# Kernel tuning notes

Measured on AMD Instinct MI355X. Metric: run time of the kernel, lower is better.

Reference implementation:

```python
import jax, jax.numpy as jnp
import numpy as np

B, N, K, Q = 2, 4096, 48, 20  # batch, nodes, neighbors, Potts states (amino acids)


def setup_inputs() -> dict:
    key = jax.random.key(0)
    k1, k2, k3, k4 = jax.random.split(key, 4)
    h = jax.random.normal(k1, (B, N, Q), dtype=jnp.float32)
    J = jax.random.normal(k2, (B, N, K, Q, Q), dtype=jnp.float32)
    edge_idx = jax.random.randint(k3, (B, N, K), 0, N)
    S = jax.random.randint(k4, (B, N), 0, Q)
    return {"S": S, "h": h, "J": J, "edge_idx": edge_idx}


def reference(S, h, J, edge_idx):
    """Potts energy: U (B,), U_i (B,N,Q). Faithful to compute_potts_energy."""
    Bs, Ns, Ks, Qs, _ = J.shape
    # collect_neighbors: S_j[b,i,k] = S[b, edge_idx[b,i,k]]
    S_j = jnp.take_along_axis(S, edge_idx.reshape(Bs, Ns * Ks), axis=1).reshape(Bs, Ns, Ks)
    # J_ij[b,i,k,q] = J[b,i,k,q, S_j[b,i,k]]  (gather along last state axis)
    idx = jnp.broadcast_to(S_j[..., None, None], (Bs, Ns, Ks, Qs, 1))
    J_ij = jnp.take_along_axis(J, idx, axis=-1)[..., 0]      # (B,N,K,Q)
    J_i = J_ij.sum(axis=2)                                    # (B,N,Q)
    U_i = h + J_i
    gather_s = lambda T: jnp.take_along_axis(T, S[..., None], axis=-1)[..., 0]  # (B,N)
    U = (gather_s(U_i) - 0.5 * gather_s(J_i)).sum(axis=1)     # (B,)
    return U, U_i
```

## Files before the change

kernel.cpp:

```cpp
#include <hip/hip_runtime.h>
#include <hip/hip_bf16.h>


constexpr int Bc = 2;
constexpr int Nc = 4096;
constexpr int Kc = 48;
constexpr int Qc = 20;
constexpr int NODE_FLOATS = Kc * Qc * Qc;
constexpr int NODE_F4     = NODE_FLOATS / 4;
constexpr int TPB         = 320;

__global__ __launch_bounds__(TPB) void potts_node_kernel(
    const int*   __restrict__ S,
    const float* __restrict__ h,
    const float* __restrict__ J,
    const int*   __restrict__ edge_idx,
    float*       __restrict__ U_i_out,
    float*       __restrict__ node_c)
{
    const int node = blockIdx.x;
    const int b    = node >> 12;
    const int tid  = threadIdx.x;

    __shared__ float Jl[Qc];
    __shared__ int   sj[Kc];
    __shared__ int   s_i_sh;

    if (tid < Qc) Jl[tid] = 0.0f;
    if (tid < Kc) {
        int e = edge_idx[node * Kc + tid];
        sj[tid] = S[b * Nc + e];
    }
    if (tid == 0) s_i_sh = S[node];
    __syncthreads();

    const float4* Jb = (const float4*)(J + (size_t)node * NODE_FLOATS);
    #pragma unroll 5
    for (int j = 0; j < NODE_F4 / TPB; ++j) {
        const int m = tid + j * TPB;
        float4 v = Jb[m];
        int k  = m / 100;
        int r  = m - k * 100;
        int q  = r / 5;
        int s0 = (r - q * 5) << 2;
        int d  = sj[k] - s0;
        if ((unsigned)d < 4u) {
            float val = (d == 0) ? v.x : (d == 1) ? v.y : (d == 2) ? v.z : v.w;
            atomicAdd(&Jl[q], val);
        }
    }
    __syncthreads();

    if (tid < Qc) {
        float ji = Jl[tid];
        float ui = h[node * Qc + tid] + ji;
        U_i_out[node * Qc + tid] = ui;
        if (tid == s_i_sh) {
            node_c[node] = ui - 0.5f * ji;
        }
    }
}

__global__ __launch_bounds__(256) void potts_reduce_kernel(
    const float* __restrict__ node_c, float* __restrict__ U)
{
    const int b   = blockIdx.x;
    const int tid = threadIdx.x;
    float s = 0.0f;
    for (int i = tid; i < Nc; i += 256) s += node_c[b * Nc + i];
    #pragma unroll
    for (int off = 32; off > 0; off >>= 1) s += __shfl_down(s, off, 64);
    __shared__ float ws[4];
    if ((tid & 63) == 0) ws[tid >> 6] = s;
    __syncthreads();
    if (tid == 0) U[b] = ws[0] + ws[1] + ws[2] + ws[3];
}

extern "C" void kernel_launch(void* const* d_in, const int* in_sizes, int n_in,
                              void* d_out, int out_size, void* d_ws, size_t ws_size,
                              hipStream_t stream) {
    const int*   S        = (const int*)  d_in[0];
    const float* h        = (const float*)d_in[1];
    const float* J        = (const float*)d_in[2];
    const int*   edge_idx = (const int*)  d_in[3];

    float* out    = (float*)d_out;
    float* U      = out;
    float* U_i    = out + Bc;
    float* node_c = (float*)d_ws;

    potts_node_kernel<<<Bc * Nc, TPB, 0, stream>>>(S, h, J, edge_idx, U_i, node_c);
    potts_reduce_kernel<<<Bc, 256, 0, stream>>>(node_c, U);
}
```

Baseline: 796.7 us.

## Split each node's neighbor stream across single-wave blocks with global atomic accumulation

Each node's J slab is now split into three groups of 16 neighbors, each handled by a 64-thread block, so there are three times as many smaller blocks to keep more loads in flight. Partial field sums are added into U_i with global atomics after a separate init kernel copies h into U_i. The final reduction is rewritten to compute the energy as 0.5*(U_i + h) at the native state, which removes the per-node workspace. The LDS atomic is now unconditional (it adds zero when not selected), which adds extra atomic traffic, and the extra launch and global atomics add overhead.

After: 901.9 us. 13.2% more time.

```diff
diff --git a/kernel.cpp b/kernel.cpp
--- a/kernel.cpp
+++ b/kernel.cpp
@@ -1,73 +1,79 @@
 #include <hip/hip_runtime.h>
-#include <hip/hip_bf16.h>
 
 
 constexpr int Bc = 2;
 constexpr int Nc = 4096;
 constexpr int Kc = 48;
 constexpr int Qc = 20;
-constexpr int NODE_FLOATS = Kc * Qc * Qc;
-constexpr int NODE_F4     = NODE_FLOATS / 4;
-constexpr int TPB         = 320;
+constexpr int KG   = 16;
+constexpr int NKG  = Kc / KG;
+constexpr int GRP_F4 = KG * Qc * Qc / 4;
+constexpr int TPB_A  = 64;
+constexpr int NITER  = GRP_F4 / TPB_A;
 
-__global__ __launch_bounds__(TPB) void potts_node_kernel(
+__global__ __launch_bounds__(256) void potts_init_kernel(
+    const float* __restrict__ h, float* __restrict__ U_i)
+{
+    const int i = blockIdx.x * 256 + threadIdx.x;
+    ((float4*)U_i)[i] = ((const float4*)h)[i];
+}
+
+__global__ __launch_bounds__(TPB_A) void potts_stream_kernel(
     const int*   __restrict__ S,
-    const float* __restrict__ h,
     const float* __restrict__ J,
     const int*   __restrict__ edge_idx,
-    float*       __restrict__ U_i_out,
-    float*       __restrict__ node_c)
+    float*       __restrict__ U_i)
 {
-    const int node = blockIdx.x;
+    const int unit = blockIdx.x;
+    const int node = unit / NKG;
+    const int kg   = unit - node * NKG;
     const int b    = node >> 12;
-    const int tid  = threadIdx.x;
+    const int lane = threadIdx.x;
 
     __shared__ float Jl[Qc];
-    __shared__ int   sj[Kc];
-    __shared__ int   s_i_sh;
+    __shared__ int   sj[KG];
 
-    if (tid < Qc) Jl[tid] = 0.0f;
-    if (tid < Kc) {
-        int e = edge_idx[node * Kc + tid];
-        sj[tid] = S[b * Nc + e];
+    if (lane < Qc) Jl[lane] = 0.0f;
+    if (lane < KG) {
+        int e = edge_idx[node * Kc + kg * KG + lane];
+        sj[lane] = S[b * Nc + e];
     }
-    if (tid == 0) s_i_sh = S[node];
     __syncthreads();
 
-    const float4* Jb = (const float4*)(J + (size_t)node * NODE_FLOATS);
-    #pragma unroll 5
-    for (int j = 0; j < NODE_F4 / TPB; ++j) {
-        const int m = tid + j * TPB;
-        float4 v = Jb[m];
+    const float4* Jf4 = (const float4*)J + (size_t)node * (Kc * Qc * Qc / 4)
+                                         + (size_t)kg * GRP_F4;
+    #pragma unroll
+    for (int i = 0; i < NITER; ++i) {
+        const int m = i * TPB_A + lane;
+        float4 v = Jf4[m];
         int k  = m / 100;
         int r  = m - k * 100;
         int q  = r / 5;
         int s0 = (r - q * 5) << 2;
         int d  = sj[k] - s0;
-        if ((unsigned)d < 4u) {
-            float val = (d == 0) ? v.x : (d == 1) ? v.y : (d == 2) ? v.z : v.w;
-            atomicAdd(&Jl[q], val);
-        }
+        float val = (d == 0) ? v.x : (d == 1) ? v.y : (d == 2) ? v.z : v.w;
+        val = ((unsigned)d < 4u) ? val : 0.0f;
+        atomicAdd(&Jl[q], val);
     }
     __syncthreads();
 
-    if (tid < Qc) {
-        float ji = Jl[tid];
-        float ui = h[node * Qc + tid] + ji;
-        U_i_out[node * Qc + tid] = ui;
-        if (tid == s_i_sh) {
-            node_c[node] = ui - 0.5f * ji;
-        }
-    }
+    if (lane < Qc) atomicAdd(&U_i[node * Qc + lane], Jl[lane]);
 }
 
 __global__ __launch_bounds__(256) void potts_reduce_kernel(
-    const float* __restrict__ node_c, float* __restrict__ U)
+    const int*   __restrict__ S,
+    const float* __restrict__ h,
+    const float* __restrict__ U_i,
+    float*       __restrict__ U)
 {
     const int b   = blockIdx.x;
     const int tid = threadIdx.x;
     float s = 0.0f;
-    for (int i = tid; i < Nc; i += 256) s += node_c[b * Nc + i];
+    for (int n = tid; n < Nc; n += 256) {
+        int st  = S[b * Nc + n];
+        int idx = (b * Nc + n) * Qc + st;
+        s += 0.5f * (U_i[idx] + h[idx]);
+    }
     #pragma unroll
     for (int off = 32; off > 0; off >>= 1) s += __shfl_down(s, off, 64);
     __shared__ float ws[4];
@@ -84,11 +90,11 @@
     const float* J        = (const float*)d_in[2];
     const int*   edge_idx = (const int*)  d_in[3];
 
-    float* out    = (float*)d_out;
-    float* U      = out;
-    float* U_i    = out + Bc;
-    float* node_c = (float*)d_ws;
+    float* out = (float*)d_out;
+    float* U   = out;
+    float* U_i = out + Bc;
 
-    potts_node_kernel<<<Bc * Nc, TPB, 0, stream>>>(S, h, J, edge_idx, U_i, node_c);
-    potts_reduce_kernel<<<Bc, 256, 0, stream>>>(node_c, U);
+    potts_init_kernel<<<Bc * Nc * Qc / 4 / 256, 256, 0, stream>>>(h, U_i);
+    potts_stream_kernel<<<Bc * Nc * NKG, TPB_A, 0, stream>>>(S, J, edge_idx, U_i);
+    potts_reduce_kernel<<<Bc, 256, 0, stream>>>(S, h, U_i, U);
 }
```

## Gather only the needed J column per neighbor instead of streaming all of J

Applied to the files above, without the earlier changes.

Replaces the full streaming read of each node's 48x20x20 J block, and the shared-memory atomics that went with it, with a targeted gather. One thread per neighbor computes S_j and reads only the 20 strided entries J[k,q,S_j]. The per-node sums are then done through a padded shared-memory transpose. Because each 4-byte read is strided and only fills part of a memory sector, most of the bandwidth of the full 768MB J stream is avoided. The cost is scattered, uncoalesced loads and only 48 of 64 lanes active.

Result: no change. 796.1 us (-0.1%).

```diff
diff --git a/kernel.cpp b/kernel.cpp
--- a/kernel.cpp
+++ b/kernel.cpp
@@ -1,5 +1,4 @@
 #include <hip/hip_runtime.h>
-#include <hip/hip_bf16.h>
 
 
 constexpr int Bc = 2;
@@ -7,10 +6,8 @@
 constexpr int Kc = 48;
 constexpr int Qc = 20;
 constexpr int NODE_FLOATS = Kc * Qc * Qc;
-constexpr int NODE_F4     = NODE_FLOATS / 4;
-constexpr int TPB         = 320;
 
-__global__ __launch_bounds__(TPB) void potts_node_kernel(
+__global__ __launch_bounds__(64) void potts_gather_kernel(
     const int*   __restrict__ S,
     const float* __restrict__ h,
     const float* __restrict__ J,
@@ -20,42 +17,31 @@
 {
     const int node = blockIdx.x;
     const int b    = node >> 12;
-    const int tid  = threadIdx.x;
+    const int l    = threadIdx.x;
 
-    __shared__ float Jl[Qc];
-    __shared__ int   sj[Kc];
-    __shared__ int   s_i_sh;
+    __shared__ float T[Kc][Qc + 1];
 
-    if (tid < Qc) Jl[tid] = 0.0f;
-    if (tid < Kc) {
-        int e = edge_idx[node * Kc + tid];
-        sj[tid] = S[b * Nc + e];
-    }
-    if (tid == 0) s_i_sh = S[node];
-    __syncthreads();
+    const int s_i = S[node];
 
-    const float4* Jb = (const float4*)(J + (size_t)node * NODE_FLOATS);
-    #pragma unroll 5
-    for (int j = 0; j < NODE_F4 / TPB; ++j) {
-        const int m = tid + j * TPB;
-        float4 v = Jb[m];
-        int k  = m / 100;
-        int r  = m - k * 100;
-        int q  = r / 5;
-        int s0 = (r - q * 5) << 2;
-        int d  = sj[k] - s0;
-        if ((unsigned)d < 4u) {
-            float val = (d == 0) ? v.x : (d == 1) ? v.y : (d == 2) ? v.z : v.w;
-            atomicAdd(&Jl[q], val);
-        }
+    if (l < Kc) {
+        const int e  = edge_idx[node * Kc + l];
+        const int sl = S[b * Nc + e];
+        const float* Jp = J + (size_t)node * NODE_FLOATS + l * (Qc * Qc) + sl;
+        float v[Qc];
+        #pragma unroll
+        for (int q = 0; q < Qc; ++q) v[q] = Jp[q * Qc];
+        #pragma unroll
+        for (int q = 0; q < Qc; ++q) T[l][q] = v[q];
     }
     __syncthreads();
 
-    if (tid < Qc) {
-        float ji = Jl[tid];
-        float ui = h[node * Qc + tid] + ji;
-        U_i_out[node * Qc + tid] = ui;
-        if (tid == s_i_sh) {
+    if (l < Qc) {
+        float ji = 0.0f;
+        #pragma unroll
+        for (int k = 0; k < Kc; ++k) ji += T[k][l];
+        const float ui = h[node * Qc + l] + ji;
+        U_i_out[node * Qc + l] = ui;
+        if (l == s_i) {
             node_c[node] = ui - 0.5f * ji;
         }
     }
@@ -89,6 +75,6 @@
     float* U_i    = out + Bc;
     float* node_c = (float*)d_ws;
 
-    potts_node_kernel<<<Bc * Nc, TPB, 0, stream>>>(S, h, J, edge_idx, U_i, node_c);
+    potts_gather_kernel<<<Bc * Nc, 64, 0, stream>>>(S, h, J, edge_idx, U_i, node_c);
     potts_reduce_kernel<<<Bc, 256, 0, stream>>>(node_c, U);
 }
```
